# Kernel optimization log

Hardware: AMD Instinct MI355X
Metric: run time of the kernel (lower is better)

Reference implementation:

```python
import jax, jax.numpy as jnp
import numpy as np

NUM_GRAPHS = 128
NODES_PER_GRAPH = 512
N_NODES = NUM_GRAPHS * NODES_PER_GRAPH
N_EDGES = 524288
IN_DIM = 128
HID = 128
OUT_DIM = 10
N_LAYERS = 3
POOL_RATIO = 0.5  # TopKPooling default ratio


def setup_inputs() -> dict:
    key = jax.random.key(0)
    ks = jax.random.split(key, 16)
    x = jax.random.normal(ks[0], (N_NODES, IN_DIM), dtype=jnp.float32)
    edge_index = jax.random.randint(ks[1], (2, N_EDGES), 0, N_NODES, dtype=jnp.int64)
    batch = jnp.repeat(jnp.arange(NUM_GRAPHS, dtype=jnp.int64), NODES_PER_GRAPH)
    s = 0.05
    return {
        "x": x,
        "edge_index": edge_index,
        "batch": batch,
        "emb_W": jax.random.normal(ks[2], (IN_DIM, HID), dtype=jnp.float32) * s,
        "emb_b": jnp.zeros((HID,), dtype=jnp.float32),
        "gcn_W": jax.random.normal(ks[3], (N_LAYERS, HID, HID), dtype=jnp.float32) * s,
        "gcn_b": jnp.zeros((N_LAYERS, HID), dtype=jnp.float32),
        "pool_p": jax.random.normal(ks[4], (HID,), dtype=jnp.float32),
        "fc1_W": jax.random.normal(ks[5], (HID, 128), dtype=jnp.float32) * s,
        "fc1_b": jnp.zeros((128,), dtype=jnp.float32),
        "fc2_W": jax.random.normal(ks[6], (128, 64), dtype=jnp.float32) * s,
        "fc2_b": jnp.zeros((64,), dtype=jnp.float32),
        "fc3_W": jax.random.normal(ks[7], (64, OUT_DIM), dtype=jnp.float32) * s,
        "fc3_b": jnp.zeros((OUT_DIM,), dtype=jnp.float32),
    }


def reference(x, edge_index, batch, emb_W, emb_b, gcn_W, gcn_b, pool_p,
              fc1_W, fc1_b, fc2_W, fc2_b, fc3_W, fc3_b):
    n = x.shape[0]
    # embedding
    h = x @ emb_W + emb_b
    # GCNConv normalization (PyG semantics): add self loops, deg from target scatter
    loop = jnp.arange(n, dtype=edge_index.dtype)
    src = jnp.concatenate([edge_index[0], loop])
    dst = jnp.concatenate([edge_index[1], loop])
    deg = jax.ops.segment_sum(jnp.ones_like(src, dtype=h.dtype), dst, num_segments=n)
    dinv = jnp.where(deg > 0, jax.lax.rsqrt(jnp.maximum(deg, 1e-12)), 0.0)
    norm = dinv[src] * dinv[dst]  # [E+n]
    for l in range(gcn_W.shape[0]):
        hw = h @ gcn_W[l]                                   # [n, HID]
        msg = hw[src] * norm[:, None]                        # gather + scale
        h = jax.nn.relu(jax.ops.segment_sum(msg, dst, num_segments=n) + gcn_b[l])
    # TopKPooling (ratio=0.5, tanh nonlinearity), uniform graphs -> reshape + top_k
    npg = n // NUM_GRAPHS
    k = int(np.ceil(POOL_RATIO * npg))
    score = (h @ pool_p) / jnp.linalg.norm(pool_p)           # [n]
    score_g = score.reshape(NUM_GRAPHS, npg)
    topv, topi = jax.lax.top_k(score_g, k)                   # [G, k]
    h_g = h.reshape(NUM_GRAPHS, npg, -1)
    h_sel = jnp.take_along_axis(h_g, topi[:, :, None], axis=1) * jnp.tanh(topv)[:, :, None]
    pooled = h_sel.mean(axis=1)                              # global_mean_pool -> [G, HID]
    # MLP head (dropout is identity in eval)
    z = jax.nn.relu(pooled @ fc1_W + fc1_b)
    z = jax.nn.relu(z @ fc2_W + fc2_b)
    return z @ fc3_W + fc3_b
```

## Files before the change

kernel.cpp:

```cpp
#include <hip/hip_runtime.h>
#include <hip/hip_bf16.h>
#include <math.h>


static __device__ __forceinline__ float4 f4add(float4 a, float4 b) {
    return make_float4(a.x + b.x, a.y + b.y, a.z + b.z, a.w + b.w);
}
static __device__ __forceinline__ float4 f4fma(float s, float4 a, float4 acc) {
    return make_float4(fmaf(s, a.x, acc.x), fmaf(s, a.y, acc.y),
                       fmaf(s, a.z, acc.z), fmaf(s, a.w, acc.w));
}

__global__ __launch_bounds__(128) void fold_emb(
    const float* __restrict__ embW, const float* __restrict__ embb,
    const float* __restrict__ W0, float* __restrict__ W01,
    float* __restrict__ b01)
{
    const int r = blockIdx.x;
    const int c = threadIdx.x;
    __shared__ float rs[128];
    rs[c] = (r < 128) ? embW[r * 128 + c] : embb[c];
    __syncthreads();
    float s = 0.f;
#pragma unroll 8
    for (int k = 0; k < 128; k++) s = fmaf(rs[k], W0[k * 128 + c], s);
    if (r < 128) W01[r * 128 + c] = s;
    else         b01[c] = s;
}

#define ASTRIDE 257
#define WSTRIDE 140
__global__ __launch_bounds__(256) void gemm128(
    const float* __restrict__ A, const float* __restrict__ W,
    const float* __restrict__ bias, const float* __restrict__ rowscale,
    float* __restrict__ out, int n)
{
    __shared__ float As[32 * ASTRIDE];
    __shared__ float Ws[32 * WSTRIDE];
    const int tid  = threadIdx.x;
    const int rb   = blockIdx.x * 128;
    const int tc   = tid & 15;
    const int tr   = tid >> 4;
    const int colg = tc * 8;
    const int cswz = colg + ((colg >> 5) << 2);
    const int rowg = tr * 8;

    const int a_kq = tid & 7;
    const int a_m  = tid >> 3;
    const int w_c  = (tid & 31) * 4;
    const int w_cs = w_c + ((w_c >> 5) << 2);
    const int w_k  = tid >> 5;

    float acc[8][8];
#pragma unroll
    for (int i = 0; i < 8; i++)
#pragma unroll
        for (int j = 0; j < 8; j++) acc[i][j] = 0.f;

    float4 areg[4], wreg[4];
#pragma unroll
    for (int t = 0; t < 4; t++)
        areg[t] = *(const float4*)&A[(size_t)(rb + t * 32 + a_m) * 128 + a_kq * 4];
#pragma unroll
    for (int t = 0; t < 4; t++)
        wreg[t] = *(const float4*)&W[(size_t)(t * 8 + w_k) * 128 + w_c];

#pragma unroll 1
    for (int k0 = 0; k0 < 128; k0 += 32) {
#pragma unroll
        for (int t = 0; t < 4; t++) {
            const int m = t * 32 + a_m;
            const float4 av = areg[t];
            As[(a_kq * 4 + 0) * ASTRIDE + m] = av.x;
            As[(a_kq * 4 + 1) * ASTRIDE + m] = av.y;
            As[(a_kq * 4 + 2) * ASTRIDE + m] = av.z;
            As[(a_kq * 4 + 3) * ASTRIDE + m] = av.w;
        }
#pragma unroll
        for (int t = 0; t < 4; t++)
            *(float4*)&Ws[(t * 8 + w_k) * WSTRIDE + w_cs] = wreg[t];
        __syncthreads();
        if (k0 < 96) {
#pragma unroll
            for (int t = 0; t < 4; t++)
                areg[t] = *(const float4*)&A[(size_t)(rb + t * 32 + a_m) * 128 + k0 + 32 + a_kq * 4];
#pragma unroll
            for (int t = 0; t < 4; t++)
                wreg[t] = *(const float4*)&W[(size_t)(k0 + 32 + t * 8 + w_k) * 128 + w_c];
        }
#pragma unroll 8
        for (int kk = 0; kk < 32; kk++) {
            float4 a0 = *(const float4*)&As[kk * ASTRIDE + rowg];
            float4 a1 = *(const float4*)&As[kk * ASTRIDE + rowg + 4];
            float4 b0 = *(const float4*)&Ws[kk * WSTRIDE + cswz];
            float4 b1 = *(const float4*)&Ws[kk * WSTRIDE + cswz + 4];
            float av[8] = {a0.x, a0.y, a0.z, a0.w, a1.x, a1.y, a1.z, a1.w};
            float bv[8] = {b0.x, b0.y, b0.z, b0.w, b1.x, b1.y, b1.z, b1.w};
#pragma unroll
            for (int i = 0; i < 8; i++)
#pragma unroll
                for (int j = 0; j < 8; j++) acc[i][j] = fmaf(av[i], bv[j], acc[i][j]);
        }
        __syncthreads();
    }

    float4 bb0 = make_float4(0.f, 0.f, 0.f, 0.f), bb1 = bb0;
    if (bias) {
        bb0 = *(const float4*)&bias[colg];
        bb1 = *(const float4*)&bias[colg + 4];
    }
#pragma unroll
    for (int i = 0; i < 8; i++) {
        const int row  = rb + rowg + i;
        const float sc = rowscale ? rowscale[row] : 1.f;
        float4 o0, o1;
        o0.x = (acc[i][0] + bb0.x) * sc;  o0.y = (acc[i][1] + bb0.y) * sc;
        o0.z = (acc[i][2] + bb0.z) * sc;  o0.w = (acc[i][3] + bb0.w) * sc;
        o1.x = (acc[i][4] + bb1.x) * sc;  o1.y = (acc[i][5] + bb1.y) * sc;
        o1.z = (acc[i][6] + bb1.z) * sc;  o1.w = (acc[i][7] + bb1.w) * sc;
        *(float4*)&out[(size_t)row * 128 + colg]     = o0;
        *(float4*)&out[(size_t)row * 128 + colg + 4] = o1;
    }
}

__global__ void count_edges(const int* __restrict__ dst, int* __restrict__ cnt, int E)
{
    int e = blockIdx.x * blockDim.x + threadIdx.x;
    if (e < E) atomicAdd(&cnt[dst[e]], 1);
}

__global__ void scan1(const int* __restrict__ cnt, int* __restrict__ offs,
                      int* __restrict__ bsum, float* __restrict__ dinv)
{
    __shared__ int tmp[256];
    int t = threadIdx.x;
    int i = blockIdx.x * 256 + t;
    int v = cnt[i];
    dinv[i] = rsqrtf((float)(v + 1));
    tmp[t] = v;
    __syncthreads();
    for (int o = 1; o < 256; o <<= 1) {
        int add = (t >= o) ? tmp[t - o] : 0;
        __syncthreads();
        tmp[t] += add;
        __syncthreads();
    }
    offs[i] = tmp[t] - v;
    if (t == 255) bsum[blockIdx.x] = tmp[255];
}

__global__ void scan2(const int* __restrict__ bsum, int* __restrict__ boff)
{
    __shared__ int tmp[256];
    int t = threadIdx.x;
    int v = bsum[t];
    tmp[t] = v;
    __syncthreads();
    for (int o = 1; o < 256; o <<= 1) {
        int add = (t >= o) ? tmp[t - o] : 0;
        __syncthreads();
        tmp[t] += add;
        __syncthreads();
    }
    boff[t] = tmp[t] - v;
}

__global__ void scan3(int* __restrict__ offs, const int* __restrict__ boff,
                      int* __restrict__ cursor, int n, int E)
{
    int i = blockIdx.x * 256 + threadIdx.x;
    int v = offs[i] + boff[blockIdx.x];
    offs[i]   = v;
    cursor[i] = v;
    if (i == 0) offs[n] = E;
}

__global__ void scatter_edges(const int* __restrict__ src, const int* __restrict__ dst,
                              int* __restrict__ cursor, int* __restrict__ csr, int E)
{
    int e = blockIdx.x * blockDim.x + threadIdx.x;
    if (e < E) {
        int d   = dst[e];
        int pos = atomicAdd(&cursor[d], 1);
        csr[pos] = src[e];
    }
}

__global__ __launch_bounds__(256) void aggregate(
    const float* __restrict__ hs, const int* __restrict__ csr,
    const int* __restrict__ offs, const float* __restrict__ dinv,
    const float* __restrict__ bias, float* __restrict__ hout,
    const float* __restrict__ pool_p, float* __restrict__ scores, int n)
{
    const int grp  = threadIdx.x >> 5;
    const int lane = threadIdx.x & 31;
    const int node = blockIdx.x * 8 + grp;
    const float4* __restrict__ hv = (const float4*)hs;

    const int e0 = offs[node], e1 = offs[node + 1];

    int   ix[16];
    float mk[16];
#pragma unroll
    for (int j = 0; j < 16; j++) {
        const int  e  = e0 + j;
        const bool v  = e < e1;
        const int  ce = v ? e : (e1 > 0 ? e1 - 1 : 0);
        ix[j] = csr[ce];
        mk[j] = v ? 1.f : 0.f;
    }

    float4 self = hv[(size_t)node * 32 + lane];
    float4 r[16];
#pragma unroll
    for (int j = 0; j < 16; j++)
        r[j] = hv[(size_t)ix[j] * 32 + lane];
    asm volatile("" ::: "memory");

    float4 a0 = self;
    float4 a1 = make_float4(0.f, 0.f, 0.f, 0.f);
    float4 a2 = a1, a3 = a1;
#pragma unroll
    for (int j = 0; j < 16; j += 4) {
        a0 = f4fma(mk[j + 0], r[j + 0], a0);
        a1 = f4fma(mk[j + 1], r[j + 1], a1);
        a2 = f4fma(mk[j + 2], r[j + 2], a2);
        a3 = f4fma(mk[j + 3], r[j + 3], a3);
    }
    for (int e = e0 + 16; e < e1; e++) {
        a1 = f4add(a1, hv[(size_t)csr[e] * 32 + lane]);
    }

    float4 s = f4add(f4add(a0, a1), f4add(a2, a3));
    const float dv = dinv[node];
    const float4 bb = ((const float4*)bias)[lane];
    float4 o;
    o.x = fmaxf(fmaf(s.x, dv, bb.x), 0.f);
    o.y = fmaxf(fmaf(s.y, dv, bb.y), 0.f);
    o.z = fmaxf(fmaf(s.z, dv, bb.z), 0.f);
    o.w = fmaxf(fmaf(s.w, dv, bb.w), 0.f);
    ((float4*)hout)[(size_t)node * 32 + lane] = o;

    if (scores) {
        float4 pv = ((const float4*)pool_p)[lane];
        float d  = o.x * pv.x + o.y * pv.y + o.z * pv.z + o.w * pv.w;
        float nn = pv.x * pv.x + pv.y * pv.y + pv.z * pv.z + pv.w * pv.w;
#pragma unroll
        for (int off = 16; off > 0; off >>= 1) {
            d  += __shfl_xor(d, off);
            nn += __shfl_xor(nn, off);
        }
        if (lane == 0) scores[node] = d * rsqrtf(nn);
    }
}

__global__ __launch_bounds__(512) void topk_pool(
    const float* __restrict__ scores, const float* __restrict__ h,
    float* __restrict__ pooled)
{
    __shared__ float s[512];
    __shared__ int   sel[256];
    __shared__ float w[256];
    __shared__ float4 red[512];
    const int g = blockIdx.x;
    const int i = threadIdx.x;
    s[i] = scores[g * 512 + i];
    __syncthreads();
    float si = s[i];
    int rank = 0;
    for (int j = 0; j < 512; j++) {
        float sj = s[j];
        rank += (sj > si) || (sj == si && j < i);
    }
    if (rank < 256) {
        sel[rank] = i;
        w[rank]   = tanhf(si) * (1.f / 256.f);
    }
    __syncthreads();
    const int c   = (i & 31) * 4;
    const int grp = i >> 5;
    float4 acc = make_float4(0.f, 0.f, 0.f, 0.f);
    for (int t = grp; t < 256; t += 16) {
        float wt  = w[t];
        int   idx = sel[t];
        float4 r = *(const float4*)&h[((size_t)g * 512 + idx) * 128 + c];
        acc = f4fma(wt, r, acc);
    }
    red[i] = acc;
    __syncthreads();
    if (i < 256) red[i] = f4add(red[i], red[i + 256]);
    __syncthreads();
    if (i < 128) red[i] = f4add(red[i], red[i + 128]);
    __syncthreads();
    if (i < 64) red[i] = f4add(red[i], red[i + 64]);
    __syncthreads();
    if (i < 32) {
        float4 v = f4add(red[i], red[i + 32]);
        *(float4*)&pooled[g * 128 + i * 4] = v;
    }
}

__global__ __launch_bounds__(128) void mlp_head(
    const float* __restrict__ pooled,
    const float* __restrict__ fc1W, const float* __restrict__ fc1b,
    const float* __restrict__ fc2W, const float* __restrict__ fc2b,
    const float* __restrict__ fc3W, const float* __restrict__ fc3b,
    float* __restrict__ out)
{
    __shared__ float pld[128];
    __shared__ float z1[128];
    __shared__ float z2[64];
    int g = blockIdx.x, j = threadIdx.x;
    pld[j] = pooled[g * 128 + j];
    __syncthreads();
    float a = fc1b[j];
    for (int k = 0; k < 128; k++) a += pld[k] * fc1W[k * 128 + j];
    z1[j] = fmaxf(a, 0.f);
    __syncthreads();
    if (j < 64) {
        float b = fc2b[j];
        for (int k = 0; k < 128; k++) b += z1[k] * fc2W[k * 64 + j];
        z2[j] = fmaxf(b, 0.f);
    }
    __syncthreads();
    if (j < 10) {
        float o = fc3b[j];
        for (int k = 0; k < 64; k++) o += z2[k] * fc3W[k * 10 + j];
        out[g * 10 + j] = o;
    }
}

extern "C" void kernel_launch(void* const* d_in, const int* in_sizes, int n_in,
                              void* d_out, int out_size, void* d_ws, size_t ws_size,
                              hipStream_t stream)
{
    const float* x     = (const float*)d_in[0];
    const int*   eidx  = (const int*)d_in[1];
    const float* embW  = (const float*)d_in[3];
    const float* embb  = (const float*)d_in[4];
    const float* gcnW  = (const float*)d_in[5];
    const float* gcnb  = (const float*)d_in[6];
    const float* poolp = (const float*)d_in[7];
    const float* fc1W  = (const float*)d_in[8];
    const float* fc1b  = (const float*)d_in[9];
    const float* fc2W  = (const float*)d_in[10];
    const float* fc2b  = (const float*)d_in[11];
    const float* fc3W  = (const float*)d_in[12];
    const float* fc3b  = (const float*)d_in[13];
    float* out = (float*)d_out;

    const int n = in_sizes[0] / 128;
    const int E = in_sizes[1] / 2;
    const int G = n / 512;

    const int* src = eidx;
    const int* dst = eidx + E;

    char* ws = (char*)d_ws;
    size_t off = 0;
    auto carve = [&](size_t bytes) {
        void* p = ws + off;
        off += (bytes + 255) & ~(size_t)255;
        return p;
    };
    float* h      = (float*)carve((size_t)n * 128 * 4);
    float* hs     = (float*)carve((size_t)n * 128 * 4);
    float* dinv   = (float*)carve((size_t)n * 4);
    int*   cnt    = (int*)carve((size_t)n * 4);
    int*   offs   = (int*)carve((size_t)(n + 1) * 4);
    int*   cursor = (int*)carve((size_t)n * 4);
    int*   bsum   = (int*)carve(256 * 4);
    int*   boff   = (int*)carve(256 * 4);
    int*   csr    = (int*)carve((size_t)E * 4);
    float* scores = (float*)carve((size_t)n * 4);
    float* pooled = (float*)carve((size_t)G * 128 * 4);
    float* W01    = (float*)carve(128 * 128 * 4);
    float* b01    = (float*)carve(128 * 4);
    (void)ws_size;

    hipMemsetAsync(cnt, 0, (size_t)n * 4, stream);
    count_edges<<<E / 256, 256, 0, stream>>>(dst, cnt, E);
    scan1<<<n / 256, 256, 0, stream>>>(cnt, offs, bsum, dinv);
    scan2<<<1, 256, 0, stream>>>(bsum, boff);
    scan3<<<n / 256, 256, 0, stream>>>(offs, boff, cursor, n, E);
    scatter_edges<<<E / 256, 256, 0, stream>>>(src, dst, cursor, csr, E);

    fold_emb<<<129, 128, 0, stream>>>(embW, embb, gcnW, W01, b01);

    gemm128<<<n / 128, 256, 0, stream>>>(x, W01, b01, dinv, hs, n);
    aggregate<<<n / 8, 256, 0, stream>>>(hs, csr, offs, dinv, gcnb, h,
                                         poolp, nullptr, n);

    for (int l = 1; l < 3; l++) {
        gemm128<<<n / 128, 256, 0, stream>>>(h, gcnW + (size_t)l * 128 * 128,
                                             nullptr, dinv, hs, n);
        aggregate<<<n / 8, 256, 0, stream>>>(
            hs, csr, offs, dinv, gcnb + (size_t)l * 128, h,
            poolp, (l == 2) ? scores : nullptr, n);
    }

    topk_pool<<<G, 512, 0, stream>>>(scores, h, pooled);
    mlp_head<<<G, 128, 0, stream>>>(pooled, fc1W, fc1b, fc2W, fc2b, fc3W, fc3b, out);
}
```

Before: 430.5 us.

## Pack GEMM FMAs, fuse scan and topk/MLP kernels, use rank-based CSR scatter

The GEMM inner product now uses two-wide float vectors with elementwise FMA so the compiler can emit packed FP32 FMA instructions. scan2 and scan3 are merged into one kernel, and topk_pool and mlp_head are merged into one, removing two launches. The CSR build records each edge's rank from the counting atomic so the scatter needs no second atomic pass. fold_emb splits its dot product across four thread groups. The cost is an extra E-sized rank buffer and a redundant 256-element block-sum scan in every scan23 block.

```diff
diff --git a/kernel.cpp b/kernel.cpp
--- a/kernel.cpp
+++ b/kernel.cpp
@@ -3,6 +3,8 @@
 #include <math.h>
 
 
+typedef __attribute__((ext_vector_type(2))) float v2f;
+
 static __device__ __forceinline__ float4 f4add(float4 a, float4 b) {
     return make_float4(a.x + b.x, a.y + b.y, a.z + b.z, a.w + b.w);
 }
@@ -11,21 +13,29 @@
                        fmaf(s, a.z, acc.z), fmaf(s, a.w, acc.w));
 }
 
-__global__ __launch_bounds__(128) void fold_emb(
+__global__ __launch_bounds__(512) void fold_emb(
     const float* __restrict__ embW, const float* __restrict__ embb,
     const float* __restrict__ W0, float* __restrict__ W01,
     float* __restrict__ b01)
 {
+    __shared__ float rs[128];
+    __shared__ float part[512];
     const int r = blockIdx.x;
-    const int c = threadIdx.x;
-    __shared__ float rs[128];
-    rs[c] = (r < 128) ? embW[r * 128 + c] : embb[c];
+    const int t = threadIdx.x;
+    const int c = t & 127, q = t >> 7;
+    if (t < 128) rs[t] = (r < 128) ? embW[r * 128 + t] : embb[t];
     __syncthreads();
     float s = 0.f;
+    const int k0 = q * 32;
 #pragma unroll 8
-    for (int k = 0; k < 128; k++) s = fmaf(rs[k], W0[k * 128 + c], s);
-    if (r < 128) W01[r * 128 + c] = s;
-    else         b01[c] = s;
+    for (int k = k0; k < k0 + 32; k++) s = fmaf(rs[k], W0[k * 128 + c], s);
+    part[t] = s;
+    __syncthreads();
+    if (q == 0) {
+        float v = (part[c] + part[c + 128]) + (part[c + 256] + part[c + 384]);
+        if (r < 128) W01[r * 128 + c] = v;
+        else         b01[c] = v;
+    }
 }
 
 #define ASTRIDE 257
@@ -51,11 +61,11 @@
     const int w_cs = w_c + ((w_c >> 5) << 2);
     const int w_k  = tid >> 5;
 
-    float acc[8][8];
+    v2f acc[8][4];
 #pragma unroll
     for (int i = 0; i < 8; i++)
 #pragma unroll
-        for (int j = 0; j < 8; j++) acc[i][j] = 0.f;
+        for (int j = 0; j < 4; j++) acc[i][j] = (v2f){0.f, 0.f};
 
     float4 areg[4], wreg[4];
 #pragma unroll
@@ -95,38 +105,44 @@
             float4 b0 = *(const float4*)&Ws[kk * WSTRIDE + cswz];
             float4 b1 = *(const float4*)&Ws[kk * WSTRIDE + cswz + 4];
             float av[8] = {a0.x, a0.y, a0.z, a0.w, a1.x, a1.y, a1.z, a1.w};
-            float bv[8] = {b0.x, b0.y, b0.z, b0.w, b1.x, b1.y, b1.z, b1.w};
-#pragma unroll
-            for (int i = 0; i < 8; i++)
-#pragma unroll
-                for (int j = 0; j < 8; j++) acc[i][j] = fmaf(av[i], bv[j], acc[i][j]);
+            v2f bv[4] = {{b0.x, b0.y}, {b0.z, b0.w}, {b1.x, b1.y}, {b1.z, b1.w}};
+#pragma unroll
+            for (int i = 0; i < 8; i++) {
+                const v2f a2 = {av[i], av[i]};
+#pragma unroll
+                for (int j = 0; j < 4; j++)
+                    acc[i][j] = __builtin_elementwise_fma(a2, bv[j], acc[i][j]);
+            }
         }
         __syncthreads();
     }
 
-    float4 bb0 = make_float4(0.f, 0.f, 0.f, 0.f), bb1 = bb0;
+    v2f bb[4] = {{0.f, 0.f}, {0.f, 0.f}, {0.f, 0.f}, {0.f, 0.f}};
     if (bias) {
-        bb0 = *(const float4*)&bias[colg];
-        bb1 = *(const float4*)&bias[colg + 4];
+        float4 t0 = *(const float4*)&bias[colg];
+        float4 t1 = *(const float4*)&bias[colg + 4];
+        bb[0] = (v2f){t0.x, t0.y}; bb[1] = (v2f){t0.z, t0.w};
+        bb[2] = (v2f){t1.x, t1.y}; bb[3] = (v2f){t1.z, t1.w};
     }
 #pragma unroll
     for (int i = 0; i < 8; i++) {
         const int row  = rb + rowg + i;
         const float sc = rowscale ? rowscale[row] : 1.f;
-        float4 o0, o1;
-        o0.x = (acc[i][0] + bb0.x) * sc;  o0.y = (acc[i][1] + bb0.y) * sc;
-        o0.z = (acc[i][2] + bb0.z) * sc;  o0.w = (acc[i][3] + bb0.w) * sc;
-        o1.x = (acc[i][4] + bb1.x) * sc;  o1.y = (acc[i][5] + bb1.y) * sc;
-        o1.z = (acc[i][6] + bb1.z) * sc;  o1.w = (acc[i][7] + bb1.w) * sc;
+        v2f o[4];
+#pragma unroll
+        for (int j = 0; j < 4; j++) o[j] = (acc[i][j] + bb[j]) * sc;
+        float4 o0 = make_float4(o[0].x, o[0].y, o[1].x, o[1].y);
+        float4 o1 = make_float4(o[2].x, o[2].y, o[3].x, o[3].y);
         *(float4*)&out[(size_t)row * 128 + colg]     = o0;
         *(float4*)&out[(size_t)row * 128 + colg + 4] = o1;
     }
 }
 
-__global__ void count_edges(const int* __restrict__ dst, int* __restrict__ cnt, int E)
+__global__ void count_edges(const int* __restrict__ dst, int* __restrict__ cnt,
+                            int* __restrict__ rank, int E)
 {
     int e = blockIdx.x * blockDim.x + threadIdx.x;
-    if (e < E) atomicAdd(&cnt[dst[e]], 1);
+    if (e < E) rank[e] = atomicAdd(&cnt[dst[e]], 1);
 }
 
 __global__ void scan1(const int* __restrict__ cnt, int* __restrict__ offs,
@@ -149,9 +165,11 @@
     if (t == 255) bsum[blockIdx.x] = tmp[255];
 }
 
-__global__ void scan2(const int* __restrict__ bsum, int* __restrict__ boff)
+__global__ void scan23(int* __restrict__ offs, const int* __restrict__ bsum,
+                       int n, int E)
 {
     __shared__ int tmp[256];
+    __shared__ int excl[256];
     int t = threadIdx.x;
     int v = bsum[t];
     tmp[t] = v;
@@ -162,28 +180,19 @@
         tmp[t] += add;
         __syncthreads();
     }
-    boff[t] = tmp[t] - v;
-}
-
-__global__ void scan3(int* __restrict__ offs, const int* __restrict__ boff,
-                      int* __restrict__ cursor, int n, int E)
-{
-    int i = blockIdx.x * 256 + threadIdx.x;
-    int v = offs[i] + boff[blockIdx.x];
-    offs[i]   = v;
-    cursor[i] = v;
+    excl[t] = tmp[t] - v;
+    __syncthreads();
+    int i = blockIdx.x * 256 + t;
+    offs[i] += excl[blockIdx.x];
     if (i == 0) offs[n] = E;
 }
 
 __global__ void scatter_edges(const int* __restrict__ src, const int* __restrict__ dst,
-                              int* __restrict__ cursor, int* __restrict__ csr, int E)
+                              const int* __restrict__ offs, const int* __restrict__ rank,
+                              int* __restrict__ csr, int E)
 {
     int e = blockIdx.x * blockDim.x + threadIdx.x;
-    if (e < E) {
-        int d   = dst[e];
-        int pos = atomicAdd(&cursor[d], 1);
-        csr[pos] = src[e];
-    }
+    if (e < E) csr[offs[dst[e]] + rank[e]] = src[e];
 }
 
 __global__ __launch_bounds__(256) void aggregate(
@@ -254,14 +263,20 @@
     }
 }
 
-__global__ __launch_bounds__(512) void topk_pool(
+__global__ __launch_bounds__(512) void topk_mlp(
     const float* __restrict__ scores, const float* __restrict__ h,
-    float* __restrict__ pooled)
+    const float* __restrict__ fc1W, const float* __restrict__ fc1b,
+    const float* __restrict__ fc2W, const float* __restrict__ fc2b,
+    const float* __restrict__ fc3W, const float* __restrict__ fc3b,
+    float* __restrict__ out)
 {
     __shared__ float s[512];
     __shared__ int   sel[256];
     __shared__ float w[256];
     __shared__ float4 red[512];
+    __shared__ float pld[128];
+    __shared__ float z1[128];
+    __shared__ float z2[64];
     const int g = blockIdx.x;
     const int i = threadIdx.x;
     s[i] = scores[g * 512 + i];
@@ -296,37 +311,25 @@
     __syncthreads();
     if (i < 32) {
         float4 v = f4add(red[i], red[i + 32]);
-        *(float4*)&pooled[g * 128 + i * 4] = v;
-    }
-}
-
-__global__ __launch_bounds__(128) void mlp_head(
-    const float* __restrict__ pooled,
-    const float* __restrict__ fc1W, const float* __restrict__ fc1b,
-    const float* __restrict__ fc2W, const float* __restrict__ fc2b,
-    const float* __restrict__ fc3W, const float* __restrict__ fc3b,
-    float* __restrict__ out)
-{
-    __shared__ float pld[128];
-    __shared__ float z1[128];
-    __shared__ float z2[64];
-    int g = blockIdx.x, j = threadIdx.x;
-    pld[j] = pooled[g * 128 + j];
-    __syncthreads();
-    float a = fc1b[j];
-    for (int k = 0; k < 128; k++) a += pld[k] * fc1W[k * 128 + j];
-    z1[j] = fmaxf(a, 0.f);
-    __syncthreads();
-    if (j < 64) {
-        float b = fc2b[j];
-        for (int k = 0; k < 128; k++) b += z1[k] * fc2W[k * 64 + j];
-        z2[j] = fmaxf(b, 0.f);
-    }
-    __syncthreads();
-    if (j < 10) {
-        float o = fc3b[j];
-        for (int k = 0; k < 64; k++) o += z2[k] * fc3W[k * 10 + j];
-        out[g * 10 + j] = o;
+        *(float4*)&pld[i * 4] = v;
+    }
+    __syncthreads();
+    if (i < 128) {
+        float a = fc1b[i];
+        for (int k = 0; k < 128; k++) a += pld[k] * fc1W[k * 128 + i];
+        z1[i] = fmaxf(a, 0.f);
+    }
+    __syncthreads();
+    if (i < 64) {
+        float b = fc2b[i];
+        for (int k = 0; k < 128; k++) b += z1[k] * fc2W[k * 64 + i];
+        z2[i] = fmaxf(b, 0.f);
+    }
+    __syncthreads();
+    if (i < 10) {
+        float o = fc3b[i];
+        for (int k = 0; k < 64; k++) o += z2[k] * fc3W[k * 10 + i];
+        out[g * 10 + i] = o;
     }
 }
 
@@ -368,24 +371,21 @@
     float* dinv   = (float*)carve((size_t)n * 4);
     int*   cnt    = (int*)carve((size_t)n * 4);
     int*   offs   = (int*)carve((size_t)(n + 1) * 4);
-    int*   cursor = (int*)carve((size_t)n * 4);
+    int*   rank   = (int*)carve((size_t)E * 4);
     int*   bsum   = (int*)carve(256 * 4);
-    int*   boff   = (int*)carve(256 * 4);
     int*   csr    = (int*)carve((size_t)E * 4);
     float* scores = (float*)carve((size_t)n * 4);
-    float* pooled = (float*)carve((size_t)G * 128 * 4);
     float* W01    = (float*)carve(128 * 128 * 4);
     float* b01    = (float*)carve(128 * 4);
     (void)ws_size;
 
     hipMemsetAsync(cnt, 0, (size_t)n * 4, stream);
-    count_edges<<<E / 256, 256, 0, stream>>>(dst, cnt, E);
+    count_edges<<<E / 256, 256, 0, stream>>>(dst, cnt, rank, E);
     scan1<<<n / 256, 256, 0, stream>>>(cnt, offs, bsum, dinv);
-    scan2<<<1, 256, 0, stream>>>(bsum, boff);
-    scan3<<<n / 256, 256, 0, stream>>>(offs, boff, cursor, n, E);
-    scatter_edges<<<E / 256, 256, 0, stream>>>(src, dst, cursor, csr, E);
-
-    fold_emb<<<129, 128, 0, stream>>>(embW, embb, gcnW, W01, b01);
+    scan23<<<n / 256, 256, 0, stream>>>(offs, bsum, n, E);
+    scatter_edges<<<E / 256, 256, 0, stream>>>(src, dst, offs, rank, csr, E);
+
+    fold_emb<<<129, 512, 0, stream>>>(embW, embb, gcnW, W01, b01);
 
     gemm128<<<n / 128, 256, 0, stream>>>(x, W01, b01, dinv, hs, n);
     aggregate<<<n / 8, 256, 0, stream>>>(hs, csr, offs, dinv, gcnb, h,
@@ -399,6 +399,6 @@
             poolp, (l == 2) ? scores : nullptr, n);
     }
 
-    topk_pool<<<G, 512, 0, stream>>>(scores, h, pooled);
-    mlp_head<<<G, 128, 0, stream>>>(pooled, fc1W, fc1b, fc2W, fc2b, fc3W, fc3b, out);
-}
+    topk_mlp<<<G, 512, 0, stream>>>(scores, h, fc1W, fc1b, fc2W, fc2b,
+                                    fc3W, fc3b, out);
+}
```

New measurement: 404.8 us. 5.9% less time.
